# Kernel tuning notes

Measured on AMD Instinct MI355X. Metric: run time of the kernel, lower is better.

The kernel has to match this reference:

```python
import jax, jax.numpy as jnp
import numpy as np

CURV = 1.0          # manifold curvature c
HEADS = 4
HEAD_DIM = 32       # (dim-1) // heads = 128 // 4
SCALE = HEAD_DIM ** -0.5
EPS = 1e-7

N_NODES = 50000
N_EDGES = 800000
D = 128             # tangent feature dim (dim - 1)


def log_origin(x, c):
    """Lorentz log map at the origin o=(1/sqrt(c),0,...); returns spatial (d) part of tangent."""
    sc = jnp.sqrt(c)
    x0 = x[..., 0]
    xs = x[..., 1:]
    norm = jnp.sqrt(jnp.sum(xs * xs, axis=-1) + EPS)         # (N,)
    dist = jnp.arccosh(jnp.maximum(sc * x0, 1.0 + EPS)) / sc  # (N,)
    return (dist / norm)[..., None] * xs                      # (N, d)


def exp_origin(vs, c):
    """Lorentz exp map at origin of tangent vector (0, vs); returns point (N, d+1)."""
    sc = jnp.sqrt(c)
    r = jnp.sqrt(jnp.sum(vs * vs, axis=-1) + EPS)  # (N,)
    arg = sc * r
    x0 = jnp.cosh(arg) / sc
    xs = (jnp.sinh(arg) / arg)[..., None] * vs
    return jnp.concatenate([x0[..., None], xs], axis=-1)


def setup_inputs() -> dict:
    key = jax.random.key(0)
    k1, k2, k3, k4, k5, k6, k7 = jax.random.split(key, 7)
    # valid hyperboloid points: x0 = sqrt(1/c + ||xs||^2)
    xs = 0.5 * jax.random.normal(k1, (N_NODES, D), dtype=jnp.float32)
    x0 = jnp.sqrt(1.0 / CURV + jnp.sum(xs * xs, axis=-1, keepdims=True))
    x = jnp.concatenate([x0, xs], axis=-1)  # (N, d+1)
    edge_index = jax.random.randint(k2, (2, N_EDGES), 0, N_NODES, dtype=jnp.int64)
    s = D ** -0.5
    Wq = s * jax.random.normal(k3, (D, D), dtype=jnp.float32)
    Wk = s * jax.random.normal(k4, (D, D), dtype=jnp.float32)
    Wv = s * jax.random.normal(k5, (D, D), dtype=jnp.float32)
    Wo = s * jax.random.normal(k6, (D, D), dtype=jnp.float32)
    bo = jnp.zeros((D,), dtype=jnp.float32)
    return {"x": x, "edge_index": edge_index, "Wq": Wq, "Wk": Wk, "Wv": Wv, "Wo": Wo, "bo": bo}


def reference(x, edge_index, Wq, Wk, Wv, Wo, bo):
    N = x.shape[0]
    row, col = edge_index[0], edge_index[1]
    # map to tangent space at origin, drop the (zero) time component
    x_tan = log_origin(x, CURV)                       # (N, d)
    Q = (x_tan @ Wq.T).reshape(N, HEADS, HEAD_DIM)
    K = (x_tan @ Wk.T).reshape(N, HEADS, HEAD_DIM)
    V = (x_tan @ Wv.T).reshape(N, HEADS, HEAD_DIM)
    # per-edge attention logits, grouped softmax over incoming edges of each target node (col)
    scores = jnp.einsum('ehd,ehd->eh', Q[col], K[row]) * SCALE   # (E, H)
    m = jax.ops.segment_max(scores, col, num_segments=N)         # (N, H)
    e = jnp.exp(scores - m[col])
    denom = jax.ops.segment_sum(e, col, num_segments=N)          # (N, H)
    att = e / denom[col]                                         # (E, H)
    # weighted scatter-sum of values
    agg = jax.ops.segment_sum(att[..., None] * V[row], col, num_segments=N)  # (N, H, hd)
    agg = agg.reshape(N, HEADS * HEAD_DIM)
    out = agg @ Wo.T + bo                                        # (N, d)
    # lift back: prepend zero time component, exp map at origin
    return exp_origin(out, CURV)                                 # (N, d+1)
```

## Files before the change

### kernel.cpp

```cpp
#include <hip/hip_runtime.h>
#include <hip/hip_fp8.h>
#include <math.h>

#define EPS 1e-7f
#define SCALE 0.17677669529663687f
#define MAXDEG 64

typedef _Float16 half2v __attribute__((ext_vector_type(2)));
typedef _Float16 f16x4 __attribute__((ext_vector_type(4)));
typedef _Float16 f16x8 __attribute__((ext_vector_type(8)));
typedef float f32x4 __attribute__((ext_vector_type(4)));

__device__ __forceinline__ void gload16(const void* g, void* l) {
  __builtin_amdgcn_global_load_lds(
      (const __attribute__((address_space(1))) unsigned int*)g,
      (__attribute__((address_space(3))) unsigned int*)l, 16, 0, 0);
}

__device__ __forceinline__ float f8tof(unsigned char u) {
  __hip_fp8_e4m3 h;
  h.__x = (__hip_fp8_storage_t)u;
  return (float)h;
}
__device__ __forceinline__ unsigned char ftof8(float f) {
  __hip_fp8_e4m3 h(f);
  return (unsigned char)h.__x;
}

__global__ __launch_bounds__(256) void prep_kernel(
    const float* __restrict__ x,
    const float* __restrict__ Wq, const float* __restrict__ Wk,
    const float* __restrict__ Wv, const float* __restrict__ Wo,
    _Float16* __restrict__ Wc, _Float16* __restrict__ Wof,
    _Float16* __restrict__ xt, int* __restrict__ cnt, int N) {
  int b = blockIdx.x;
  if (b < 256) {
    int o = b * 256 + threadIdx.x;
    int j = o >> 7;
    int i = o & 127;
    if (j < 384) {
      const float* W = (j < 128) ? Wq : (j < 256) ? Wk : Wv;
      Wc[o] = (_Float16)W[(j & 127) * 128 + i];
    } else {
      Wof[(j - 384) * 128 + i] = (_Float16)Wo[(j - 384) * 128 + i];
    }
    return;
  }
  int node = (b - 256) * 4 + (threadIdx.x >> 6);
  if (node >= N) return;
  int lane = threadIdx.x & 63;
  float2 xs = *reinterpret_cast<const float2*>(&x[(size_t)node * 129 + 1 + lane * 2]);
  float ss = fmaf(xs.x, xs.x, xs.y * xs.y);
#pragma unroll
  for (int o = 32; o >= 1; o >>= 1) ss += __shfl_xor(ss, o, 64);
  float norm = sqrtf(ss + EPS);
  float x0 = x[(size_t)node * 129];
  float dist = acoshf(fmaxf(x0, 1.0f + EPS));
  float sc = dist / norm;
  half2v h;
  h.x = (_Float16)(sc * xs.x);
  h.y = (_Float16)(sc * xs.y);
  *reinterpret_cast<half2v*>(&xt[(size_t)node * 128 + lane * 2]) = h;
  if (lane == 0) cnt[node] = 0;
}

template <int NCHUNKS, int MODE>
__global__ __launch_bounds__(256, 3) void gemm_mfma(
    const _Float16* __restrict__ A,
    const _Float16* __restrict__ B,
    void* __restrict__ C0, void* __restrict__ C1,
    const float* __restrict__ bias, int M,
    const int* __restrict__ col, const int* __restrict__ row,
    int* __restrict__ cnt, unsigned short* __restrict__ rml, int E) {
  int bid;
  if (MODE == 0) {
    if ((blockIdx.x & 1) == 0) {
      int stride = (gridDim.x >> 1) * 256;
      for (int e = (blockIdx.x >> 1) * 256 + (int)threadIdx.x; e < E; e += stride) {
        int c = col[e];
        int pos = atomicAdd(&cnt[c], 1);
        if (pos < MAXDEG) rml[(size_t)c * MAXDEG + pos] = (unsigned short)row[e];
      }
      return;
    }
    bid = blockIdx.x >> 1;
  } else {
    bid = blockIdx.x;
  }

  __shared__ _Float16 Bs[128 * 128];
  __shared__ __align__(16) unsigned char Cs[16384];
  const int tid = threadIdx.x;
  const int wave = tid >> 6;
  const int lane = tid & 63;
  const int wm = wave >> 1, wn = wave & 1;
  const int lrow = lane & 15, q = lane >> 4;
  const int m0 = bid * 64;

#pragma unroll
  for (int j = 0; j < 4; j++) {
    int slot0 = (j * 4 + wave) * 64;
    int p = slot0 + lane;
    int m = p >> 4;
    int kcl = (p & 15) ^ (m & 15);
    int msrc = m0 + m;
    if (msrc > M - 1) msrc = M - 1;
    gload16(A + (size_t)msrc * 128 + kcl * 8, (char*)Bs + (size_t)slot0 * 16);
  }
  __syncthreads();

  f16x8 afr[2][4];
  {
    const f16x8* Av = (const f16x8*)Bs;
#pragma unroll
    for (int mt = 0; mt < 2; mt++) {
      int m = wm * 32 + mt * 16 + lrow;
#pragma unroll
      for (int s = 0; s < 4; s++) {
        int kc = s * 4 + q;
        afr[mt][s] = Av[m * 16 + (kc ^ (m & 15))];
      }
    }
  }
  __syncthreads();

  auto stageB = [&](int c) {
#pragma unroll
    for (int j = 0; j < 8; j++) {
      int slot0 = (j * 4 + wave) * 64;
      int p = slot0 + lane;
      int n = p >> 4;
      int kcl = (p & 15) ^ (n & 15);
      gload16(B + ((size_t)(c * 128 + n)) * 128 + kcl * 8, (char*)Bs + (size_t)slot0 * 16);
    }
  };
  stageB(0);

  f32x4 acc[2][4];
  for (int c = 0; c < NCHUNKS; c++) {
    __syncthreads();

#pragma unroll
    for (int mt = 0; mt < 2; mt++)
#pragma unroll
      for (int nt = 0; nt < 4; nt++) acc[mt][nt] = (f32x4)0.f;

    const f16x8* Bv = (const f16x8*)Bs;
#pragma unroll
    for (int s = 0; s < 4; s++) {
      int kc = s * 4 + q;
      f16x8 bf[4];
#pragma unroll
      for (int nt = 0; nt < 4; nt++) {
        int n = wn * 64 + nt * 16 + lrow;
        bf[nt] = Bv[n * 16 + (kc ^ (n & 15))];
      }
#pragma unroll
      for (int mt = 0; mt < 2; mt++)
#pragma unroll
        for (int nt = 0; nt < 4; nt++)
          acc[mt][nt] = __builtin_amdgcn_mfma_f32_16x16x32_f16(afr[mt][s], bf[nt], acc[mt][nt], 0, 0, 0);
    }

    if (MODE == 0) {
      if (c == 0) {
#pragma unroll
        for (int mt = 0; mt < 2; mt++)
#pragma unroll
          for (int reg = 0; reg < 4; reg++) {
            int r = wm * 32 + mt * 16 + q * 4 + reg;
            int sw = ((r >> 2) & 3) << 5;
#pragma unroll
            for (int nt = 0; nt < 4; nt++) {
              int cl = wn * 64 + nt * 16 + lrow;
              *(_Float16*)(Cs + r * 256 + ((cl * 2) ^ sw)) = (_Float16)acc[mt][nt][reg];
            }
          }
      } else {
        unsigned char* cb = Cs + ((c == 2) ? 8192 : 0);
#pragma unroll
        for (int mt = 0; mt < 2; mt++)
#pragma unroll
          for (int reg = 0; reg < 4; reg++) {
            int r = wm * 32 + mt * 16 + q * 4 + reg;
            int sw = ((r >> 2) & 3) << 5;
#pragma unroll
            for (int nt = 0; nt < 4; nt++) {
              int cl = wn * 64 + nt * 16 + lrow;
              cb[r * 128 + (cl ^ sw)] = ftof8(acc[mt][nt][reg]);
            }
          }
      }
    }
    __syncthreads();
    if (c + 1 < NCHUNKS) stageB(c + 1);
    if (MODE == 0) {
      if (c == 0) {
#pragma unroll
        for (int it = 0; it < 4; it++) {
          int off = it * 4096 + tid * 16;
          int r = off >> 8;
          int bo = off & 255;
          int sw = ((r >> 2) & 3) << 5;
          uint4 v = *(const uint4*)(Cs + r * 256 + (bo ^ sw));
          int rg = m0 + r;
          if (rg < M) *(uint4*)((char*)C0 + (size_t)rg * 256 + bo) = v;
        }
      } else if (c == 2) {
#pragma unroll
        for (int it = 0; it < 8; it++) {
          int off = it * 2048 + tid * 8;
          int r = off >> 8;
          int u4 = (off & 255) >> 1;
          int sw = ((r >> 2) & 3) << 5;
          unsigned kw = *(const unsigned*)(Cs + r * 128 + (u4 ^ sw));
          unsigned vw = *(const unsigned*)(Cs + 8192 + r * 128 + (u4 ^ sw));
          int rg = m0 + r;
          if (rg < M) {
            uint2 o;
            o.x = kw;
            o.y = vw;
            *(uint2*)((char*)C1 + (size_t)rg * 256 + (off & 255)) = o;
          }
        }
      }
    }
  }

  if (MODE == 1) {
    float* out = (float*)C0;
    float* rsum = (float*)Cs;
#pragma unroll
    for (int mt = 0; mt < 2; mt++)
#pragma unroll
      for (int nt = 0; nt < 4; nt++) {
        int cl = wn * 64 + nt * 16 + lrow;
        float b = bias[cl];
#pragma unroll
        for (int reg = 0; reg < 4; reg++) acc[mt][nt][reg] += b;
      }
#pragma unroll
    for (int mt = 0; mt < 2; mt++) {
#pragma unroll
      for (int reg = 0; reg < 4; reg++) {
        float s4 = 0.f;
#pragma unroll
        for (int nt = 0; nt < 4; nt++) s4 = fmaf(acc[mt][nt][reg], acc[mt][nt][reg], s4);
#pragma unroll
        for (int o = 8; o >= 1; o >>= 1) s4 += __shfl_xor(s4, o, 16);
        if (lrow == 0) rsum[(wm * 32 + mt * 16 + q * 4 + reg) * 2 + wn] = s4;
      }
    }
    __syncthreads();
#pragma unroll
    for (int mt = 0; mt < 2; mt++) {
#pragma unroll
      for (int reg = 0; reg < 4; reg++) {
        int rl = wm * 32 + mt * 16 + q * 4 + reg;
        int rg = m0 + rl;
        if (rg < M) {
          float tot = rsum[rl * 2] + rsum[rl * 2 + 1];
          float r = sqrtf(tot + EPS);
          float s = sinhf(r) / r;
#pragma unroll
          for (int nt = 0; nt < 4; nt++) {
            int cl = wn * 64 + nt * 16 + lrow;
            out[(size_t)rg * 129 + 1 + cl] = s * acc[mt][nt][reg];
          }
          if (wn == 0 && lrow == 0) out[(size_t)rg * 129] = coshf(r);
        }
      }
    }
  }
}

__global__ __launch_bounds__(256) void attn_kernel(
    const _Float16* __restrict__ Qb,
    const unsigned char* __restrict__ KVI,
    const unsigned short* __restrict__ rml, const int* __restrict__ cnt,
    _Float16* __restrict__ agg, int N) {
  int node = blockIdx.x * 4 + (threadIdx.x >> 6);
  if (node >= N) return;
  int lane = threadIdx.x & 63;
  int par = lane >> 5;
  int hd = lane & 31;
  int qoff = hd * 4;
  f16x4 qh = *reinterpret_cast<const f16x4*>(Qb + (size_t)node * 128 + qoff);
  float q0 = (float)qh[0], q1 = (float)qh[1], q2 = (float)qh[2], q3 = (float)qh[3];
  int deg = cnt[node];
  if (deg > MAXDEG) deg = MAXDEG;
  const unsigned short* el = rml + (size_t)node * MAXDEG;
  float l = 0.f, av0 = 0.f, av1 = 0.f, av2 = 0.f, av3 = 0.f;

  auto dot = [&](uint2 w, float& p, float& v0, float& v1, float& v2, float& v3) {
    unsigned kx = w.x, vx = w.y;
    float k0 = f8tof(kx & 255), k1 = f8tof((kx >> 8) & 255);
    float k2 = f8tof((kx >> 16) & 255), k3 = f8tof(kx >> 24);
    v0 = f8tof(vx & 255); v1 = f8tof((vx >> 8) & 255);
    v2 = f8tof((vx >> 16) & 255); v3 = f8tof(vx >> 24);
    p = fmaf(q0, k0, fmaf(q1, k1, fmaf(q2, k2, q3 * k3)));
  };

  int i = 0;
  for (; i + 8 <= deg; i += 8) {
    int rA = el[i + par], rB = el[i + 2 + par], rC = el[i + 4 + par], rD = el[i + 6 + par];
    uint2 wA = *reinterpret_cast<const uint2*>(KVI + (size_t)rA * 256 + hd * 8);
    uint2 wB = *reinterpret_cast<const uint2*>(KVI + (size_t)rB * 256 + hd * 8);
    uint2 wC = *reinterpret_cast<const uint2*>(KVI + (size_t)rC * 256 + hd * 8);
    uint2 wD = *reinterpret_cast<const uint2*>(KVI + (size_t)rD * 256 + hd * 8);
    float pA, a4, a5, a6, a7;
    float pB, b4, b5, b6, b7;
    float pC, c4, c5, c6, c7;
    float pD, d4, d5, d6, d7;
    dot(wA, pA, a4, a5, a6, a7);
    dot(wB, pB, b4, b5, b6, b7);
    dot(wC, pC, c4, c5, c6, c7);
    dot(wD, pD, d4, d5, d6, d7);
#pragma unroll
    for (int o = 4; o >= 1; o >>= 1) {
      pA += __shfl_xor(pA, o, 8);
      pB += __shfl_xor(pB, o, 8);
      pC += __shfl_xor(pC, o, 8);
      pD += __shfl_xor(pD, o, 8);
    }
    float eA = __expf(pA * SCALE);
    float eB = __expf(pB * SCALE);
    float eC = __expf(pC * SCALE);
    float eD = __expf(pD * SCALE);
    l += (eA + eB) + (eC + eD);
    av0 = fmaf(eA, a4, av0); av0 = fmaf(eB, b4, av0);
    av1 = fmaf(eA, a5, av1); av1 = fmaf(eB, b5, av1);
    av2 = fmaf(eA, a6, av2); av2 = fmaf(eB, b6, av2);
    av3 = fmaf(eA, a7, av3); av3 = fmaf(eB, b7, av3);
    av0 = fmaf(eC, c4, av0); av0 = fmaf(eD, d4, av0);
    av1 = fmaf(eC, c5, av1); av1 = fmaf(eD, d5, av1);
    av2 = fmaf(eC, c6, av2); av2 = fmaf(eD, d6, av2);
    av3 = fmaf(eC, c7, av3); av3 = fmaf(eD, d7, av3);
  }
  for (; i + 2 <= deg; i += 2) {
    int rA = el[i + par];
    uint2 wA = *reinterpret_cast<const uint2*>(KVI + (size_t)rA * 256 + hd * 8);
    float pA, a4, a5, a6, a7;
    dot(wA, pA, a4, a5, a6, a7);
#pragma unroll
    for (int o = 4; o >= 1; o >>= 1) pA += __shfl_xor(pA, o, 8);
    float eA = __expf(pA * SCALE);
    l += eA;
    av0 = fmaf(eA, a4, av0);
    av1 = fmaf(eA, a5, av1);
    av2 = fmaf(eA, a6, av2);
    av3 = fmaf(eA, a7, av3);
  }
  if (i < deg) {
    int r = el[i];
    uint2 wA = *reinterpret_cast<const uint2*>(KVI + (size_t)r * 256 + hd * 8);
    float pA, a4, a5, a6, a7;
    dot(wA, pA, a4, a5, a6, a7);
#pragma unroll
    for (int o = 4; o >= 1; o >>= 1) pA += __shfl_xor(pA, o, 8);
    float e = __expf(pA * SCALE) * (par ? 0.f : 1.f);
    l += e;
    av0 = fmaf(e, a4, av0);
    av1 = fmaf(e, a5, av1);
    av2 = fmaf(e, a6, av2);
    av3 = fmaf(e, a7, av3);
  }
  l += __shfl_xor(l, 32, 64);
  av0 += __shfl_xor(av0, 32, 64);
  av1 += __shfl_xor(av1, 32, 64);
  av2 += __shfl_xor(av2, 32, 64);
  av3 += __shfl_xor(av3, 32, 64);
  if (par == 0) {
    float inv = (l > 0.f) ? 1.0f / l : 0.f;
    f16x4 o4;
    o4[0] = (_Float16)(av0 * inv);
    o4[1] = (_Float16)(av1 * inv);
    o4[2] = (_Float16)(av2 * inv);
    o4[3] = (_Float16)(av3 * inv);
    *reinterpret_cast<f16x4*>(agg + (size_t)node * 128 + qoff) = o4;
  }
}

extern "C" void kernel_launch(void* const* d_in, const int* in_sizes, int n_in,
                              void* d_out, int out_size, void* d_ws, size_t ws_size,
                              hipStream_t stream) {
  const float* x = (const float*)d_in[0];
  const int* ei = (const int*)d_in[1];
  const float* Wq = (const float*)d_in[2];
  const float* Wk = (const float*)d_in[3];
  const float* Wv = (const float*)d_in[4];
  const float* Wo = (const float*)d_in[5];
  const float* bo = (const float*)d_in[6];
  float* out = (float*)d_out;

  const int N = in_sizes[0] / 129;
  const int E = in_sizes[1] / 2;
  const int* row = ei;
  const int* col = ei + E;

  char* ws = (char*)d_ws;
  size_t off = 0;
  auto alloc = [&](size_t bytes) -> void* {
    off = (off + 255) & ~(size_t)255;
    void* p = ws + off;
    off += bytes;
    return p;
  };
  _Float16* xtan = (_Float16*)alloc((size_t)N * 128 * 2);
  _Float16* qbuf = (_Float16*)alloc((size_t)N * 128 * 2);
  unsigned char* kvi = (unsigned char*)alloc((size_t)N * 256);
  unsigned short* rml = (unsigned short*)alloc((size_t)N * MAXDEG * 2);
  _Float16* Wc   = (_Float16*)alloc(384 * 128 * 2);
  _Float16* Wof  = (_Float16*)alloc(128 * 128 * 2);
  int* cnt       = (int*)alloc((size_t)(N + 1) * 4);

  const int gemm_nb = (N + 63) / 64;

  prep_kernel<<<256 + (N + 3) / 4, 256, 0, stream>>>(x, Wq, Wk, Wv, Wo, Wc, Wof,
                                                     xtan, cnt, N);
  gemm_mfma<3, 0><<<gemm_nb * 2, 256, 0, stream>>>(xtan, Wc, qbuf, kvi, nullptr, N,
                                                   col, row, cnt, rml, E);
  attn_kernel<<<(N + 3) / 4, 256, 0, stream>>>(qbuf, kvi, rml, cnt, xtan, N);
  gemm_mfma<1, 1><<<gemm_nb, 256, 0, stream>>>(xtan, Wof, out, nullptr, bo, N,
                                               nullptr, nullptr, nullptr, nullptr, 0);
}
```

Measured before the change: 195.6 us.

## Move edge scatter into prep kernel with batched atomics and separate zeroing

Moves the edge-to-adjacency-list scatter (atomic slot claim plus rml write) out of the QKV GEMM kernel and into the prep kernel, using 512 blocks that each handle 8 edges per thread, with loads, atomics and stores batched so more memory operations are in flight. Counter zeroing moves to a new small kernel launched first, because the scatter now runs in the same kernel that used to zero the counters. The QKV GEMM loses its interleaved scatter blocks and now runs only GEMM tiles. This adds an extra kernel launch, and the scatter now overlaps the cheap prep work instead of the GEMM.

```diff
diff --git a/kernel.cpp b/kernel.cpp
--- a/kernel.cpp
+++ b/kernel.cpp
@@ -5,6 +5,7 @@
 #define EPS 1e-7f
 #define SCALE 0.17677669529663687f
 #define MAXDEG 64
+#define SCAT_BLOCKS 512
 
 typedef _Float16 half2v __attribute__((ext_vector_type(2)));
 typedef _Float16 f16x4 __attribute__((ext_vector_type(4)));
@@ -25,6 +26,15 @@
 __device__ __forceinline__ unsigned char ftof8(float f) {
   __hip_fp8_e4m3 h(f);
   return (unsigned char)h.__x;
+}
+
+__global__ __launch_bounds__(256) void zero_cnt(int* __restrict__ cnt, int n4) {
+  int i = blockIdx.x * 256 + threadIdx.x;
+  if (i < n4) {
+    int4 z;
+    z.x = 0; z.y = 0; z.z = 0; z.w = 0;
+    reinterpret_cast<int4*>(cnt)[i] = z;
+  }
 }
 
 __global__ __launch_bounds__(256) void prep_kernel(
@@ -32,8 +42,31 @@
     const float* __restrict__ Wq, const float* __restrict__ Wk,
     const float* __restrict__ Wv, const float* __restrict__ Wo,
     _Float16* __restrict__ Wc, _Float16* __restrict__ Wof,
-    _Float16* __restrict__ xt, int* __restrict__ cnt, int N) {
+    _Float16* __restrict__ xt, int* __restrict__ cnt,
+    const int* __restrict__ col, const int* __restrict__ row,
+    unsigned short* __restrict__ rml, int E, int N) {
   int b = blockIdx.x;
+  if (b < SCAT_BLOCKS) {
+    const int T = SCAT_BLOCKS * 256;
+    int t = b * 256 + (int)threadIdx.x;
+    int cols[8], rows[8], pos[8];
+#pragma unroll
+    for (int j = 0; j < 8; j++) {
+      int e = t + j * T;
+      bool ok = (e < E);
+      cols[j] = ok ? col[e] : -1;
+      rows[j] = ok ? row[e] : 0;
+    }
+#pragma unroll
+    for (int j = 0; j < 8; j++)
+      if (cols[j] >= 0) pos[j] = atomicAdd(&cnt[cols[j]], 1);
+#pragma unroll
+    for (int j = 0; j < 8; j++)
+      if (cols[j] >= 0 && pos[j] < MAXDEG)
+        rml[(size_t)cols[j] * MAXDEG + pos[j]] = (unsigned short)rows[j];
+    return;
+  }
+  b -= SCAT_BLOCKS;
   if (b < 256) {
     int o = b * 256 + threadIdx.x;
     int j = o >> 7;
@@ -61,7 +94,6 @@
   h.x = (_Float16)(sc * xs.x);
   h.y = (_Float16)(sc * xs.y);
   *reinterpret_cast<half2v*>(&xt[(size_t)node * 128 + lane * 2]) = h;
-  if (lane == 0) cnt[node] = 0;
 }
 
 template <int NCHUNKS, int MODE>
@@ -69,24 +101,8 @@
     const _Float16* __restrict__ A,
     const _Float16* __restrict__ B,
     void* __restrict__ C0, void* __restrict__ C1,
-    const float* __restrict__ bias, int M,
-    const int* __restrict__ col, const int* __restrict__ row,
-    int* __restrict__ cnt, unsigned short* __restrict__ rml, int E) {
-  int bid;
-  if (MODE == 0) {
-    if ((blockIdx.x & 1) == 0) {
-      int stride = (gridDim.x >> 1) * 256;
-      for (int e = (blockIdx.x >> 1) * 256 + (int)threadIdx.x; e < E; e += stride) {
-        int c = col[e];
-        int pos = atomicAdd(&cnt[c], 1);
-        if (pos < MAXDEG) rml[(size_t)c * MAXDEG + pos] = (unsigned short)row[e];
-      }
-      return;
-    }
-    bid = blockIdx.x >> 1;
-  } else {
-    bid = blockIdx.x;
-  }
+    const float* __restrict__ bias, int M) {
+  const int bid = blockIdx.x;
 
   __shared__ _Float16 Bs[128 * 128];
   __shared__ __align__(16) unsigned char Cs[16384];
@@ -412,15 +428,15 @@
   unsigned short* rml = (unsigned short*)alloc((size_t)N * MAXDEG * 2);
   _Float16* Wc   = (_Float16*)alloc(384 * 128 * 2);
   _Float16* Wof  = (_Float16*)alloc(128 * 128 * 2);
-  int* cnt       = (int*)alloc((size_t)(N + 1) * 4);
+  int* cnt       = (int*)alloc((size_t)(N + 4) * 4);
 
   const int gemm_nb = (N + 63) / 64;
 
-  prep_kernel<<<256 + (N + 3) / 4, 256, 0, stream>>>(x, Wq, Wk, Wv, Wo, Wc, Wof,
-                                                     xtan, cnt, N);
-  gemm_mfma<3, 0><<<gemm_nb * 2, 256, 0, stream>>>(xtan, Wc, qbuf, kvi, nullptr, N,
-                                                   col, row, cnt, rml, E);
+  const int n4 = (N + 4) / 4;
+  zero_cnt<<<(n4 + 255) / 256, 256, 0, stream>>>(cnt, n4);
+  prep_kernel<<<SCAT_BLOCKS + 256 + (N + 3) / 4, 256, 0, stream>>>(
+      x, Wq, Wk, Wv, Wo, Wc, Wof, xtan, cnt, col, row, rml, E, N);
+  gemm_mfma<3, 0><<<gemm_nb, 256, 0, stream>>>(xtan, Wc, qbuf, kvi, nullptr, N);
   attn_kernel<<<(N + 3) / 4, 256, 0, stream>>>(qbuf, kvi, rml, cnt, xtan, N);
-  gemm_mfma<1, 1><<<gemm_nb, 256, 0, stream>>>(xtan, Wof, out, nullptr, bo, N,
-                                               nullptr, nullptr, nullptr, nullptr, 0);
-}
+  gemm_mfma<1, 1><<<gemm_nb, 256, 0, stream>>>(xtan, Wof, out, nullptr, bo, N);
+}
```

Result: slower. 206.0 us (+5.4%).

## Replace global atomic adjacency build with two-pass bucketed binning in LDS

Applied to the files above, without the earlier changes.

Edges are first binned by destination-node bucket (256 nodes each) in the prep kernel. Each block uses a shared-memory histogram and one global atomic per bucket. Dedicated blocks in the QKV GEMM launch then build each bucket's per-node row list in LDS with shared atomics and write it out with coalesced stores. This replaces the per-edge global atomics and scattered 2-byte writes, at the cost of a staging buffer, an extra zeroing launch, and a hard cap of BUCK_CAP edges per bucket.

```diff
diff --git a/kernel.cpp b/kernel.cpp
--- a/kernel.cpp
+++ b/kernel.cpp
@@ -5,6 +5,10 @@
 #define EPS 1e-7f
 #define SCALE 0.17677669529663687f
 #define MAXDEG 64
+#define BIN_EPT 16
+#define BIN_EDGES 4096
+#define BUCK_CAP 5120
+#define NBUCK_MAX 256
 
 typedef _Float16 half2v __attribute__((ext_vector_type(2)));
 typedef _Float16 f16x4 __attribute__((ext_vector_type(4)));
@@ -25,6 +29,11 @@
 __device__ __forceinline__ unsigned char ftof8(float f) {
   __hip_fp8_e4m3 h(f);
   return (unsigned char)h.__x;
+}
+
+__global__ __launch_bounds__(256) void zero_cnt(int* __restrict__ bcnt, int n) {
+  int i = blockIdx.x * 256 + threadIdx.x;
+  if (i < n) bcnt[i] = 0;
 }
 
 __global__ __launch_bounds__(256) void prep_kernel(
@@ -32,10 +41,52 @@
     const float* __restrict__ Wq, const float* __restrict__ Wk,
     const float* __restrict__ Wv, const float* __restrict__ Wo,
     _Float16* __restrict__ Wc, _Float16* __restrict__ Wof,
-    _Float16* __restrict__ xt, int* __restrict__ cnt, int N) {
+    _Float16* __restrict__ xt,
+    const int* __restrict__ col, const int* __restrict__ row,
+    unsigned* __restrict__ staging, int* __restrict__ bcnt,
+    int bin_nb, int nbuck, int E, int N) {
+  __shared__ int hist[NBUCK_MAX];
+  __shared__ int rbase[NBUCK_MAX];
   int b = blockIdx.x;
+  int tid = threadIdx.x;
+  if (b < bin_nb) {
+    int e0 = b * BIN_EDGES;
+    if (tid < nbuck) hist[tid] = 0;
+    __syncthreads();
+    int bkt[BIN_EPT], rk[BIN_EPT];
+    unsigned pk[BIN_EPT];
+#pragma unroll
+    for (int j = 0; j < BIN_EPT; j++) {
+      int e = e0 + j * 256 + tid;
+      if (e < E) {
+        int c = col[e];
+        int r = row[e];
+        int bb = c >> 8;
+        bkt[j] = bb;
+        pk[j] = ((unsigned)(c & 255) << 16) | (unsigned)r;
+        rk[j] = atomicAdd(&hist[bb], 1);
+      } else {
+        bkt[j] = -1;
+        rk[j] = 0;
+        pk[j] = 0;
+      }
+    }
+    __syncthreads();
+    if (tid < nbuck) rbase[tid] = atomicAdd(&bcnt[tid], hist[tid]);
+    __syncthreads();
+#pragma unroll
+    for (int j = 0; j < BIN_EPT; j++) {
+      if (bkt[j] >= 0) {
+        int slot = rbase[bkt[j]] + rk[j];
+        if (slot < BUCK_CAP)
+          staging[(size_t)bkt[j] * BUCK_CAP + slot] = pk[j];
+      }
+    }
+    return;
+  }
+  b -= bin_nb;
   if (b < 256) {
-    int o = b * 256 + threadIdx.x;
+    int o = b * 256 + tid;
     int j = o >> 7;
     int i = o & 127;
     if (j < 384) {
@@ -46,9 +97,9 @@
     }
     return;
   }
-  int node = (b - 256) * 4 + (threadIdx.x >> 6);
+  int node = (b - 256) * 4 + (tid >> 6);
   if (node >= N) return;
-  int lane = threadIdx.x & 63;
+  int lane = tid & 63;
   float2 xs = *reinterpret_cast<const float2*>(&x[(size_t)node * 129 + 1 + lane * 2]);
   float ss = fmaf(xs.x, xs.x, xs.y * xs.y);
 #pragma unroll
@@ -61,7 +112,6 @@
   h.x = (_Float16)(sc * xs.x);
   h.y = (_Float16)(sc * xs.y);
   *reinterpret_cast<half2v*>(&xt[(size_t)node * 128 + lane * 2]) = h;
-  if (lane == 0) cnt[node] = 0;
 }
 
 template <int NCHUNKS, int MODE>
@@ -70,27 +120,38 @@
     const _Float16* __restrict__ B,
     void* __restrict__ C0, void* __restrict__ C1,
     const float* __restrict__ bias, int M,
-    const int* __restrict__ col, const int* __restrict__ row,
-    int* __restrict__ cnt, unsigned short* __restrict__ rml, int E) {
-  int bid;
-  if (MODE == 0) {
-    if ((blockIdx.x & 1) == 0) {
-      int stride = (gridDim.x >> 1) * 256;
-      for (int e = (blockIdx.x >> 1) * 256 + (int)threadIdx.x; e < E; e += stride) {
-        int c = col[e];
-        int pos = atomicAdd(&cnt[c], 1);
-        if (pos < MAXDEG) rml[(size_t)c * MAXDEG + pos] = (unsigned short)row[e];
-      }
-      return;
-    }
-    bid = blockIdx.x >> 1;
-  } else {
-    bid = blockIdx.x;
-  }
-
+    const unsigned* __restrict__ staging, const int* __restrict__ bcnt,
+    unsigned short* __restrict__ rml, int* __restrict__ cnt, int Mblocks) {
   __shared__ _Float16 Bs[128 * 128];
   __shared__ __align__(16) unsigned char Cs[16384];
+  const int bid = blockIdx.x;
   const int tid = threadIdx.x;
+
+  if (MODE == 0 && bid >= Mblocks) {
+    int bk = bid - Mblocks;
+    unsigned short* slab = (unsigned short*)Bs;
+    int* lc = (int*)Cs;
+    lc[tid] = 0;
+    __syncthreads();
+    int ec = bcnt[bk];
+    if (ec > BUCK_CAP) ec = BUCK_CAP;
+    const unsigned* sg = staging + (size_t)bk * BUCK_CAP;
+    for (int i = tid; i < ec; i += 256) {
+      unsigned p = sg[i];
+      int nl = p >> 16;
+      int pos = atomicAdd(&lc[nl], 1);
+      if (pos < MAXDEG) slab[nl * MAXDEG + pos] = (unsigned short)(p & 0xFFFF);
+    }
+    __syncthreads();
+    uint4* gs = (uint4*)(rml + (size_t)bk * 256 * MAXDEG);
+    const uint4* ls = (const uint4*)slab;
+#pragma unroll
+    for (int i = 0; i < 8; i++) gs[i * 256 + tid] = ls[i * 256 + tid];
+    int c = lc[tid];
+    cnt[bk * 256 + tid] = (c > MAXDEG) ? MAXDEG : c;
+    return;
+  }
+
   const int wave = tid >> 6;
   const int lane = tid & 63;
   const int wm = wave >> 1, wn = wave & 1;
@@ -398,6 +459,9 @@
   const int* row = ei;
   const int* col = ei + E;
 
+  const int nbuck = (N + 255) >> 8;
+  const int bin_nb = (E + BIN_EDGES - 1) / BIN_EDGES;
+
   char* ws = (char*)d_ws;
   size_t off = 0;
   auto alloc = [&](size_t bytes) -> void* {
@@ -409,18 +473,22 @@
   _Float16* xtan = (_Float16*)alloc((size_t)N * 128 * 2);
   _Float16* qbuf = (_Float16*)alloc((size_t)N * 128 * 2);
   unsigned char* kvi = (unsigned char*)alloc((size_t)N * 256);
-  unsigned short* rml = (unsigned short*)alloc((size_t)N * MAXDEG * 2);
-  _Float16* Wc   = (_Float16*)alloc(384 * 128 * 2);
-  _Float16* Wof  = (_Float16*)alloc(128 * 128 * 2);
-  int* cnt       = (int*)alloc((size_t)(N + 1) * 4);
+  unsigned short* rml = (unsigned short*)alloc((size_t)nbuck * 256 * MAXDEG * 2);
+  int* cnt        = (int*)alloc((size_t)nbuck * 256 * 4);
+  unsigned* staging = (unsigned*)alloc((size_t)nbuck * BUCK_CAP * 4);
+  int* bcnt       = (int*)alloc((size_t)nbuck * 4);
+  _Float16* Wc    = (_Float16*)alloc(384 * 128 * 2);
+  _Float16* Wof   = (_Float16*)alloc(128 * 128 * 2);
 
   const int gemm_nb = (N + 63) / 64;
 
-  prep_kernel<<<256 + (N + 3) / 4, 256, 0, stream>>>(x, Wq, Wk, Wv, Wo, Wc, Wof,
-                                                     xtan, cnt, N);
-  gemm_mfma<3, 0><<<gemm_nb * 2, 256, 0, stream>>>(xtan, Wc, qbuf, kvi, nullptr, N,
-                                                   col, row, cnt, rml, E);
+  zero_cnt<<<(nbuck + 255) / 256, 256, 0, stream>>>(bcnt, nbuck);
+  prep_kernel<<<bin_nb + 256 + (N + 3) / 4, 256, 0, stream>>>(
+      x, Wq, Wk, Wv, Wo, Wc, Wof, xtan, col, row, staging, bcnt, bin_nb, nbuck,
+      E, N);
+  gemm_mfma<3, 0><<<gemm_nb + nbuck, 256, 0, stream>>>(
+      xtan, Wc, qbuf, kvi, nullptr, N, staging, bcnt, rml, cnt, gemm_nb);
   attn_kernel<<<(N + 3) / 4, 256, 0, stream>>>(qbuf, kvi, rml, cnt, xtan, N);
-  gemm_mfma<1, 1><<<gemm_nb, 256, 0, stream>>>(xtan, Wof, out, nullptr, bo, N,
-                                               nullptr, nullptr, nullptr, nullptr, 0);
-}
+  gemm_mfma<1, 1><<<gemm_nb, 256, 0, stream>>>(
+      xtan, Wof, out, nullptr, bo, N, nullptr, nullptr, nullptr, nullptr, 0);
+}
```

New measurement: 175.1 us. 1.12x faster.
